# Performance work log

Measured on AMD Instinct MI355X. Metric: run time of the kernel, lower is better.

Reference implementation:

```python
import jax, jax.numpy as jnp
import numpy as np

NOISE_EPS = 1e-2   # Shazeer noisy-gating stddev floor
LN_EPS = 1e-6
LOSS_COEF = 0.01
K = 2              # num_activated_experts


def _layer_norm(x, w, b):
    mu = jnp.mean(x, axis=-1, keepdims=True)
    var = jnp.var(x, axis=-1, keepdims=True)
    return (x - mu) * jax.lax.rsqrt(var + LN_EPS) * w + b


def _cv_squared(v):
    return jnp.var(v) / (jnp.mean(v) ** 2 + 1e-10)


def _normal_cdf(z):
    return 0.5 * (1.0 + jax.scipy.special.erf(z / jnp.sqrt(jnp.asarray(2.0, z.dtype))))


def setup_inputs() -> dict:
    key = jax.random.key(0)
    ks = jax.random.split(key, 8)
    N, D, H, O, E = 8192, 512, 1024, 512, 8
    x = jax.random.normal(ks[0], (N, D), jnp.float32)
    x_offsets = jnp.sort(jax.random.randint(ks[1], (17,), 0, N)).astype(jnp.int64)
    noise = jax.random.normal(ks[2], (N, E), jnp.float32)
    s = 0.02
    return {
        "x": x,
        "x_offsets": x_offsets,
        "max_seq_len": 2048,
        "noise": noise,
        "norm_w": jnp.ones((D,), jnp.float32),
        "norm_bias": jnp.zeros((D,), jnp.float32),
        "w_gate": jax.random.normal(ks[3], (D, E), jnp.float32) * s,
        "w_noise": jax.random.normal(ks[4], (D, E), jnp.float32) * s,
        "W1": jax.random.normal(ks[5], (E, H, D), jnp.float32) * s,  # [E, model_d, input]
        "b1": jnp.zeros((E, H), jnp.float32),
        "W2": jax.random.normal(ks[6], (E, O, H), jnp.float32) * s,  # [E, output, model_d]
        "b2": jnp.zeros((E, O), jnp.float32),
        "output_weight": jax.random.normal(ks[7], (D, O), jnp.float32) * s,
    }


def reference(x, x_offsets, max_seq_len, noise, norm_w, norm_bias, w_gate, w_noise,
              W1, b1, W2, b2, output_weight):
    N, D = x.shape
    E = w_gate.shape[1]
    k_plus = min(K + 1, E)

    # pre-norm
    x_norm = _layer_norm(x, norm_w, norm_bias)

    # noisy top-k gating (training path)
    clean_logits = x_norm @ w_gate                      # [N, E]
    noise_stddev = jax.nn.softplus(x_norm @ w_noise) + NOISE_EPS
    noisy_logits = clean_logits + noise * noise_stddev

    top_logits, top_indices = jax.lax.top_k(noisy_logits, k_plus)   # [N, k+1]
    top_k_logits = top_logits[:, :K]
    top_k_indices = top_indices[:, :K]
    top_k_gates = jax.nn.softmax(top_k_logits, axis=-1)             # [N, K]

    rows = jnp.arange(N)[:, None]
    gates = jnp.zeros((N, E), top_k_gates.dtype).at[rows, top_k_indices].set(top_k_gates)

    # load = prob each expert is in top-k under the gating noise (Shazeer)
    flat = top_logits.reshape(-1)
    pos_in = jnp.arange(N) * k_plus + K
    thr_in = flat[pos_in][:, None]          # (k+1)-th value: threshold if already in
    thr_out = flat[pos_in - 1][:, None]     # k-th value: threshold if currently out
    is_in = noisy_logits > thr_in
    prob_in = _normal_cdf((clean_logits - thr_in) / noise_stddev)
    prob_out = _normal_cdf((clean_logits - thr_out) / noise_stddev)
    load_probs = jnp.where(is_in, prob_in, prob_out)                # [N, E]

    loss = LOSS_COEF * (_cv_squared(gates.sum(0)) + _cv_squared(load_probs.sum(0)))

    # dispatch stats: tokens per expert
    lengths = jnp.zeros((E,), jnp.float32).at[top_k_indices.reshape(-1)].add(1.0)
    load = lengths / lengths.sum()

    # grouped expert MLP (dense one-hot combine; gates are 0 for unrouted experts)
    h = jnp.einsum('nd,ehd->neh', x_norm, W1) + b1                  # [N, E, H]
    a = jax.nn.silu(h)
    y_e = jnp.einsum('neh,eoh->neo', a, W2) + b2                    # [N, E, O]
    y_moe = jnp.einsum('ne,neo->no', gates, y_e)                    # [N, O]

    # shared expert: addmm(y, shared_x=x, output_weight)
    y = y_moe + x @ output_weight
    return y, loss, load
```

## Files before the change

### kernel.cpp

```cpp
#include <hip/hip_runtime.h>
#include <math.h>

typedef unsigned short u16;
typedef unsigned int u32;

#define N_ROWS 8192
#define DDIM 512
#define HDIM 1024
#define ODIM 512
#define NEXP 8
#define MAXPAIRS (N_ROWS * 2)
#define MAXPOS (MAXPAIRS + NEXP * 128)
#define MAXTILES (MAXPOS / 128)

#define SM_CNT 0
#define SM_CUR 8
#define SM_AOFF 16
#define SM_GSUM 32
#define SM_LSUM 40
#define SM_WORDS 64

using short8 = __attribute__((ext_vector_type(8))) short;
using float4v = __attribute__((ext_vector_type(4))) float;

__device__ __forceinline__ u16 f2bf(float f) {
    union { float f; u32 u; } v; v.f = f;
    u32 u = v.u;
    return (u16)((u + 0x7fffu + ((u >> 16) & 1u)) >> 16);
}

__device__ __forceinline__ void async_copy16(u16* lds, const u16* g) {
    __builtin_amdgcn_global_load_lds(
        (const __attribute__((address_space(1))) void*)g,
        (__attribute__((address_space(3))) void*)lds, 16, 0, 0);
}

#define CONV_BLOCKS 8192
__global__ __launch_bounds__(256) void prep_kernel(
    const float* __restrict__ W1, const float* __restrict__ W2, const float* __restrict__ ow,
    u16* __restrict__ W1b, u16* __restrict__ W2b, u16* __restrict__ owT,
    int* __restrict__ small, int* __restrict__ bucket_rows, float* __restrict__ zeropage)
{
    __shared__ float tile[32][33];
    int b = blockIdx.x, tid = threadIdx.x;
    if (b < CONV_BLOCKS) {
        const size_t n4 = (size_t)NEXP * HDIM * DDIM / 4;
        size_t i = (size_t)b * 256 + tid;
        const float* src; u16* dst;
        if (i < n4) { src = W1; dst = W1b; } else { src = W2; dst = W2b; i -= n4; }
        float4 v = ((const float4*)src)[i];
        ushort4 o;
        o.x = f2bf(v.x); o.y = f2bf(v.y); o.z = f2bf(v.z); o.w = f2bf(v.w);
        ((ushort4*)dst)[i] = o;
    } else if (b < CONV_BLOCKS + 256) {
        int t = b - CONV_BLOCKS;
        int bx = (t & 15) * 32, by = (t >> 4) * 32;
        int tx = tid & 31, ty = tid >> 5;
        for (int r = ty; r < 32; r += 8) tile[r][tx] = ow[(size_t)(by + r) * ODIM + bx + tx];
        __syncthreads();
        for (int r = ty; r < 32; r += 8) owT[(size_t)(bx + r) * DDIM + by + tx] = f2bf(tile[tx][r]);
    } else {
        int i = (b - CONV_BLOCKS - 256) * 256 + tid;
        if (i < SM_WORDS) small[i] = 0;
        if (i < 512) zeropage[i] = 0.f;
        if (i < MAXPOS) bucket_rows[i] = -1;
    }
}

__global__ __launch_bounds__(256) void gating_kernel(
    const float* __restrict__ x, const float* __restrict__ noise,
    const float* __restrict__ norm_w, const float* __restrict__ norm_b,
    const float* __restrict__ w_gate, const float* __restrict__ w_noise,
    u16* __restrict__ xnorm_bf, u16* __restrict__ x_bf,
    int* __restrict__ pair_expert, float* __restrict__ pair_gate,
    int* __restrict__ small)
{
    __shared__ float wgT[NEXP * DDIM];
    __shared__ float wnT[NEXP * DDIM];
    __shared__ float blk_g[NEXP];
    __shared__ float blk_l[NEXP];
    __shared__ int blk_c[NEXP];
    float* smf = (float*)small;

    int tid = threadIdx.x;
    for (int i = tid; i < NEXP * DDIM; i += 256) {
        int d = i >> 3, e = i & 7;
        wgT[e * DDIM + d] = w_gate[i];
        wnT[e * DDIM + d] = w_noise[i];
    }
    if (tid < NEXP) { blk_g[tid] = 0.f; blk_l[tid] = 0.f; blk_c[tid] = 0; }
    __syncthreads();

    int wave = tid >> 6, lane = tid & 63;
    float nw[8], nb[8];
#pragma unroll
    for (int j = 0; j < 8; j++) { nw[j] = norm_w[j * 64 + lane]; nb[j] = norm_b[j * 64 + lane]; }

    for (int r = 0; r < 4; ++r) {
        int row = blockIdx.x * 16 + wave * 4 + r;
        const float* xr = x + (size_t)row * DDIM;
        float xv[8], s = 0.f, s2 = 0.f;
#pragma unroll
        for (int j = 0; j < 8; j++) { float v = xr[j * 64 + lane]; xv[j] = v; s += v; s2 += v * v; }
#pragma unroll
        for (int o = 32; o; o >>= 1) { s += __shfl_xor(s, o, 64); s2 += __shfl_xor(s2, o, 64); }
        float mu = s * (1.f / DDIM);
        float var = s2 * (1.f / DDIM) - mu * mu;
        float rstd = rsqrtf(var + 1e-6f);

        float acc[16];
#pragma unroll
        for (int e = 0; e < 16; e++) acc[e] = 0.f;
#pragma unroll
        for (int j = 0; j < 8; j++) {
            float v = (xv[j] - mu) * rstd * nw[j] + nb[j];
            int d = j * 64 + lane;
            xnorm_bf[(size_t)row * DDIM + d] = f2bf(v);
            x_bf[(size_t)row * DDIM + d] = f2bf(xv[j]);
#pragma unroll
            for (int e = 0; e < 8; e++) {
                acc[e] += v * wgT[e * DDIM + d];
                acc[8 + e] += v * wnT[e * DDIM + d];
            }
        }
#pragma unroll
        for (int e = 0; e < 16; e++)
#pragma unroll
            for (int o = 32; o; o >>= 1) acc[e] += __shfl_xor(acc[e], o, 64);

        float cl[8], sd[8], nz[8];
#pragma unroll
        for (int e = 0; e < 8; e++) {
            cl[e] = acc[e];
            float t = acc[8 + e];
            float sp = fmaxf(t, 0.f) + log1pf(expf(-fabsf(t)));
            sd[e] = sp + 0.01f;
            nz[e] = cl[e] + noise[(size_t)row * NEXP + e] * sd[e];
        }
        int idx[3]; float val[3]; u32 msk = 0;
#pragma unroll
        for (int t = 0; t < 3; t++) {
            float best = -INFINITY; int bi = 0;
#pragma unroll
            for (int e = 0; e < 8; e++)
                if (!((msk >> e) & 1) && nz[e] > best) { best = nz[e]; bi = e; }
            idx[t] = bi; val[t] = best; msk |= 1u << bi;
        }
        float e1 = expf(val[1] - val[0]);
        float g0 = 1.f / (1.f + e1), g1 = e1 / (1.f + e1);
        float thr_in = val[2], thr_out = val[1];

        if (lane == 0) {
            pair_expert[row * 2] = idx[0]; pair_gate[row * 2] = g0;
            pair_expert[row * 2 + 1] = idx[1]; pair_gate[row * 2 + 1] = g1;
            atomicAdd(&blk_g[idx[0]], g0); atomicAdd(&blk_g[idx[1]], g1);
            atomicAdd(&blk_c[idx[0]], 1); atomicAdd(&blk_c[idx[1]], 1);
#pragma unroll
            for (int e = 0; e < 8; e++) {
                float thr = (nz[e] > thr_in) ? thr_in : thr_out;
                float z = (cl[e] - thr) / sd[e];
                float p = 0.5f * (1.f + erff(z * 0.70710678118654752f));
                atomicAdd(&blk_l[e], p);
            }
        }
    }
    __syncthreads();
    if (tid < NEXP) {
        atomicAdd(smf + SM_GSUM + tid, blk_g[tid]);
        atomicAdd(smf + SM_LSUM + tid, blk_l[tid]);
        atomicAdd(&small[SM_CNT + tid], blk_c[tid]);
    }
}

__global__ __launch_bounds__(256) void scatter_kernel(
    const int* __restrict__ pair_expert, const float* __restrict__ pair_gate,
    int* __restrict__ small, int* __restrict__ bucket_rows, float* __restrict__ gate_by_pos,
    float* __restrict__ out_loss, float* __restrict__ out_load)
{
    __shared__ int aoff[NEXP + 1];
    __shared__ int blk_cnt[NEXP];
    __shared__ int blk_base[NEXP];
    int tid = threadIdx.x;
    if (tid == 0) {
        int acc = 0; aoff[0] = 0;
        for (int e = 0; e < NEXP; e++) { acc += (small[SM_CNT + e] + 127) & ~127; aoff[e + 1] = acc; }
    }
    if (tid < NEXP) blk_cnt[tid] = 0;
    __syncthreads();
    int p = blockIdx.x * 256 + tid;
    int e = pair_expert[p];
    int local = atomicAdd(&blk_cnt[e], 1);
    __syncthreads();
    if (tid < NEXP)
        blk_base[tid] = aoff[tid] + atomicAdd(&small[SM_CUR + tid], blk_cnt[tid]);
    if (blockIdx.x == 0 && tid < NEXP + 1) small[SM_AOFF + tid] = aoff[tid];
    __syncthreads();
    int pos = blk_base[e] + local;
    bucket_rows[pos] = p >> 1;
    gate_by_pos[pos] = pair_gate[p];

    if (blockIdx.x == 0 && tid == 0) {
        const float* gs = (const float*)small + SM_GSUM;
        const float* ls = (const float*)small + SM_LSUM;
        float cv[2];
        for (int t = 0; t < 2; t++) {
            const float* v = t ? ls : gs;
            float m = 0.f;
            for (int k = 0; k < NEXP; k++) m += v[k];
            m *= (1.f / NEXP);
            float var = 0.f;
            for (int k = 0; k < NEXP; k++) { float d = v[k] - m; var += d * d; }
            var *= (1.f / NEXP);
            cv[t] = var / (m * m + 1e-10f);
        }
        out_loss[0] = 0.01f * (cv[0] + cv[1]);
        int tot = 0;
        for (int k = 0; k < NEXP; k++) tot += small[SM_CNT + k];
        float inv = 1.f / (float)tot;
        for (int k = 0; k < NEXP; k++) out_load[k] = (float)small[SM_CNT + k] * inv;
    }
}

__global__ __launch_bounds__(256) void gemmA_kernel(
    const u16* __restrict__ xnorm, const u16* __restrict__ xbf,
    const u16* __restrict__ W1b, const u16* __restrict__ owT,
    const int* __restrict__ bucket_rows, const int* __restrict__ small,
    const float* __restrict__ b1, const u16* __restrict__ zeropage,
    u16* __restrict__ a_buf, float* __restrict__ y)
{
    constexpr int KD = 512;
    __shared__ __align__(16) u16 As[128 * 32];
    __shared__ __align__(16) u16 Bs[128 * 32];

    int tid = threadIdx.x;
    bool m0 = blockIdx.y < 8;
    int base, bn, e = 0;
    const u16* Bsel;
    if (m0) {
        base = blockIdx.x * 128;
        if (base >= small[SM_AOFF + 8]) return;
        while (e < 7 && base >= small[SM_AOFF + e + 1]) ++e;
        bn = blockIdx.y * 128;
        Bsel = W1b + (size_t)e * HDIM * KD;
    } else {
        int j = (blockIdx.y - 8) * 136 + blockIdx.x;
        if (j >= 256) return;
        base = (j >> 2) * 128;
        bn = (j & 3) * 128;
        Bsel = owT;
    }

    int wave = tid >> 6, lane = tid & 63;
    const int trow = wave * 32 + (lane >> 2);
    const int kcol = (lane & 3) * 8;
    const u16 *ga0, *ga1;
    if (m0) {
        int r0 = bucket_rows[base + trow];
        int r1 = bucket_rows[base + trow + 16];
        ga0 = ((r0 < 0) ? zeropage : xnorm + (size_t)r0 * KD) + kcol;
        ga1 = ((r1 < 0) ? zeropage : xnorm + (size_t)r1 * KD) + kcol;
    } else {
        ga0 = xbf + (size_t)(base + trow) * KD + kcol;
        ga1 = xbf + (size_t)(base + trow + 16) * KD + kcol;
    }
    const u16* gb0 = Bsel + (size_t)(bn + trow) * KD + kcol;
    const u16* gb1 = Bsel + (size_t)(bn + trow + 16) * KD + kcol;
    u16* lA0 = &As[(wave * 32) * 32];
    u16* lA1 = &As[(wave * 32 + 16) * 32];
    u16* lB0 = &Bs[(wave * 32) * 32];
    u16* lB1 = &Bs[(wave * 32 + 16) * 32];

    int wm = (wave & 1) * 64, wn = (wave >> 1) * 64;
    int fr = lane & 15, kg = (lane >> 4) * 8;

    float4v acc[4][4];
#pragma unroll
    for (int i = 0; i < 4; i++)
#pragma unroll
        for (int j = 0; j < 4; j++) acc[i][j] = (float4v){0.f, 0.f, 0.f, 0.f};

    for (int k0 = 0; k0 < KD; k0 += 32) {
        __syncthreads();
        async_copy16(lA0, ga0 + k0);
        async_copy16(lA1, ga1 + k0);
        async_copy16(lB0, gb0 + k0);
        async_copy16(lB1, gb1 + k0);
        __syncthreads();
        short8 af[4], bf[4];
#pragma unroll
        for (int mt = 0; mt < 4; mt++) af[mt] = *(const short8*)&As[(wm + mt * 16 + fr) * 32 + kg];
#pragma unroll
        for (int nt = 0; nt < 4; nt++) bf[nt] = *(const short8*)&Bs[(wn + nt * 16 + fr) * 32 + kg];
#pragma unroll
        for (int mt = 0; mt < 4; mt++)
#pragma unroll
            for (int nt = 0; nt < 4; nt++)
                acc[mt][nt] = __builtin_amdgcn_mfma_f32_16x16x32_bf16(af[mt], bf[nt], acc[mt][nt], 0, 0, 0);
    }

    int rbase = (lane >> 4) * 4, c16 = lane & 15;
#pragma unroll
    for (int nt = 0; nt < 4; nt++) {
        int gn = bn + wn + nt * 16 + c16;
        float bv = m0 ? b1[e * HDIM + gn] : 0.f;
#pragma unroll
        for (int mt = 0; mt < 4; mt++) {
            int gm = base + wm + mt * 16 + rbase;
#pragma unroll
            for (int r = 0; r < 4; r++) {
                float v = acc[mt][nt][r];
                if (m0) {
                    float h = v + bv;
                    float a = h * __builtin_amdgcn_rcpf(1.f + __expf(-h));
                    a_buf[(size_t)(gm + r) * HDIM + gn] = f2bf(a);
                } else {
                    y[(size_t)(gm + r) * ODIM + gn] = v;
                }
            }
        }
    }
}

__global__ __launch_bounds__(256) void gemmB_kernel(
    const u16* __restrict__ a_buf, const u16* __restrict__ W2b,
    const int* __restrict__ bucket_rows, const int* __restrict__ small,
    const float* __restrict__ b2, const float* __restrict__ gate_by_pos,
    float* __restrict__ y)
{
    constexpr int KD = 1024;
    __shared__ __align__(16) u16 As[128 * 32];
    __shared__ __align__(16) u16 Bs[128 * 32];

    int tid = threadIdx.x;
    int base = blockIdx.x * 128;
    if (base >= small[SM_AOFF + 8]) return;
    int e = 0;
    while (e < 7 && base >= small[SM_AOFF + e + 1]) ++e;
    int bn = blockIdx.y * 128;

    int wave = tid >> 6, lane = tid & 63;
    const int trow = wave * 32 + (lane >> 2);
    const int kcol = (lane & 3) * 8;
    const u16* ga0 = a_buf + (size_t)(base + trow) * KD + kcol;
    const u16* ga1 = a_buf + (size_t)(base + trow + 16) * KD + kcol;
    const u16* Bsel = W2b + (size_t)e * ODIM * KD;
    const u16* gb0 = Bsel + (size_t)(bn + trow) * KD + kcol;
    const u16* gb1 = Bsel + (size_t)(bn + trow + 16) * KD + kcol;
    u16* lA0 = &As[(wave * 32) * 32];
    u16* lA1 = &As[(wave * 32 + 16) * 32];
    u16* lB0 = &Bs[(wave * 32) * 32];
    u16* lB1 = &Bs[(wave * 32 + 16) * 32];

    int wm = (wave & 1) * 64, wn = (wave >> 1) * 64;
    int fr = lane & 15, kg = (lane >> 4) * 8;

    float4v acc[4][4];
#pragma unroll
    for (int i = 0; i < 4; i++)
#pragma unroll
        for (int j = 0; j < 4; j++) acc[i][j] = (float4v){0.f, 0.f, 0.f, 0.f};

    for (int k0 = 0; k0 < KD; k0 += 32) {
        __syncthreads();
        async_copy16(lA0, ga0 + k0);
        async_copy16(lA1, ga1 + k0);
        async_copy16(lB0, gb0 + k0);
        async_copy16(lB1, gb1 + k0);
        __syncthreads();
        short8 af[4], bf[4];
#pragma unroll
        for (int mt = 0; mt < 4; mt++) af[mt] = *(const short8*)&As[(wm + mt * 16 + fr) * 32 + kg];
#pragma unroll
        for (int nt = 0; nt < 4; nt++) bf[nt] = *(const short8*)&Bs[(wn + nt * 16 + fr) * 32 + kg];
#pragma unroll
        for (int mt = 0; mt < 4; mt++)
#pragma unroll
            for (int nt = 0; nt < 4; nt++)
                acc[mt][nt] = __builtin_amdgcn_mfma_f32_16x16x32_bf16(af[mt], bf[nt], acc[mt][nt], 0, 0, 0);
    }

    int rbase = (lane >> 4) * 4, c16 = lane & 15;
#pragma unroll
    for (int mt = 0; mt < 4; mt++) {
        int pos0 = base + wm + mt * 16 + rbase;
        int rows[4]; float gs[4];
#pragma unroll
        for (int r = 0; r < 4; r++) { rows[r] = bucket_rows[pos0 + r]; gs[r] = gate_by_pos[pos0 + r]; }
#pragma unroll
        for (int nt = 0; nt < 4; nt++) {
            int gn = bn + wn + nt * 16 + c16;
            float b2v = b2[e * ODIM + gn];
#pragma unroll
            for (int r = 0; r < 4; r++) {
                if (rows[r] >= 0)
                    unsafeAtomicAdd(&y[(size_t)rows[r] * ODIM + gn], gs[r] * (acc[mt][nt][r] + b2v));
            }
        }
    }
}

extern "C" void kernel_launch(void* const* d_in, const int* in_sizes, int n_in,
                              void* d_out, int out_size, void* d_ws, size_t ws_size,
                              hipStream_t stream)
{
    (void)in_sizes; (void)n_in; (void)out_size; (void)ws_size;
    const float* x = (const float*)d_in[0];
    const float* noise = (const float*)d_in[3];
    const float* norm_w = (const float*)d_in[4];
    const float* norm_b = (const float*)d_in[5];
    const float* w_gate = (const float*)d_in[6];
    const float* w_noise = (const float*)d_in[7];
    const float* W1 = (const float*)d_in[8];
    const float* b1 = (const float*)d_in[9];
    const float* W2 = (const float*)d_in[10];
    const float* b2 = (const float*)d_in[11];
    const float* ow = (const float*)d_in[12];

    float* y = (float*)d_out;
    float* out_loss = y + (size_t)N_ROWS * ODIM;
    float* out_load = out_loss + 1;

    char* ws = (char*)d_ws;
    size_t off = 0;
    auto alloc = [&](size_t b) { size_t p = off; off = (off + b + 255) & ~(size_t)255; return p; };
    u16* xnorm_bf = (u16*)(ws + alloc((size_t)N_ROWS * DDIM * 2));
    u16* x_bf     = (u16*)(ws + alloc((size_t)N_ROWS * DDIM * 2));
    u16* W1b      = (u16*)(ws + alloc((size_t)NEXP * HDIM * DDIM * 2));
    u16* W2b      = (u16*)(ws + alloc((size_t)NEXP * ODIM * HDIM * 2));
    u16* owT      = (u16*)(ws + alloc((size_t)DDIM * ODIM * 2));
    u16* a_buf    = (u16*)(ws + alloc((size_t)MAXPOS * HDIM * 2));
    int* pair_expert = (int*)(ws + alloc((size_t)MAXPAIRS * 4));
    float* pair_gate = (float*)(ws + alloc((size_t)MAXPAIRS * 4));
    float* gate_by_pos = (float*)(ws + alloc((size_t)MAXPOS * 4));
    int* bucket_rows = (int*)(ws + alloc((size_t)MAXPOS * 4));
    int* small       = (int*)(ws + alloc(SM_WORDS * 4));
    float* zeropage  = (float*)(ws + alloc(2048));

    prep_kernel<<<CONV_BLOCKS + 256 + 68, 256, 0, stream>>>(W1, W2, ow, W1b, W2b, owT,
                                                            small, bucket_rows, zeropage);
    gating_kernel<<<N_ROWS / 16, 256, 0, stream>>>(x, noise, norm_w, norm_b, w_gate, w_noise,
                                                   xnorm_bf, x_bf, pair_expert, pair_gate, small);
    scatter_kernel<<<MAXPAIRS / 256, 256, 0, stream>>>(pair_expert, pair_gate, small,
                                                       bucket_rows, gate_by_pos, out_loss, out_load);
    gemmA_kernel<<<dim3(MAXTILES, 10), 256, 0, stream>>>(xnorm_bf, x_bf, W1b, owT, bucket_rows,
                                                         small, b1, (const u16*)zeropage, a_buf, y);
    gemmB_kernel<<<dim3(MAXTILES, ODIM / 128), 256, 0, stream>>>(a_buf, W2b, bucket_rows, small,
                                                                 b2, gate_by_pos, y);
}
```

Measured before the change: 278.3 us.

## Load GEMM operands directly from global memory into registers, drop LDS staging

Both expert GEMM kernels stop staging A and B tiles through shared memory with async global-to-LDS copies and barriers. Each wave now loads its MFMA fragments straight from global memory into registers, with the k-loop unrolled by four. This removes the two barriers per k-step and the LDS round trip. In exchange, each wave re-fetches operands that were shared across waves, which raises global/L2 traffic and replaces coalesced 16-byte loads with per-lane strided row loads.

```diff
diff --git a/kernel.cpp b/kernel.cpp
--- a/kernel.cpp
+++ b/kernel.cpp
@@ -27,12 +27,6 @@
     union { float f; u32 u; } v; v.f = f;
     u32 u = v.u;
     return (u16)((u + 0x7fffu + ((u >> 16) & 1u)) >> 16);
-}
-
-__device__ __forceinline__ void async_copy16(u16* lds, const u16* g) {
-    __builtin_amdgcn_global_load_lds(
-        (const __attribute__((address_space(1))) void*)g,
-        (__attribute__((address_space(3))) void*)lds, 16, 0, 0);
 }
 
 #define CONV_BLOCKS 8192
@@ -221,6 +215,25 @@
     }
 }
 
+template <int KD>
+__device__ __forceinline__ void gemm_core_reg(const u16* const aptr[4], const u16* const bptr[4],
+                                              float4v acc[4][4])
+{
+#pragma unroll 4
+    for (int k0 = 0; k0 < KD; k0 += 32) {
+        short8 af[4], bf[4];
+#pragma unroll
+        for (int mt = 0; mt < 4; mt++) af[mt] = *(const short8*)(aptr[mt] + k0);
+#pragma unroll
+        for (int nt = 0; nt < 4; nt++) bf[nt] = *(const short8*)(bptr[nt] + k0);
+#pragma unroll
+        for (int mt = 0; mt < 4; mt++)
+#pragma unroll
+            for (int nt = 0; nt < 4; nt++)
+                acc[mt][nt] = __builtin_amdgcn_mfma_f32_16x16x32_bf16(af[mt], bf[nt], acc[mt][nt], 0, 0, 0);
+    }
+}
+
 __global__ __launch_bounds__(256) void gemmA_kernel(
     const u16* __restrict__ xnorm, const u16* __restrict__ xbf,
     const u16* __restrict__ W1b, const u16* __restrict__ owT,
@@ -229,9 +242,6 @@
     u16* __restrict__ a_buf, float* __restrict__ y)
 {
     constexpr int KD = 512;
-    __shared__ __align__(16) u16 As[128 * 32];
-    __shared__ __align__(16) u16 Bs[128 * 32];
-
     int tid = threadIdx.x;
     bool m0 = blockIdx.y < 8;
     int base, bn, e = 0;
@@ -251,52 +261,31 @@
     }
 
     int wave = tid >> 6, lane = tid & 63;
-    const int trow = wave * 32 + (lane >> 2);
-    const int kcol = (lane & 3) * 8;
-    const u16 *ga0, *ga1;
-    if (m0) {
-        int r0 = bucket_rows[base + trow];
-        int r1 = bucket_rows[base + trow + 16];
-        ga0 = ((r0 < 0) ? zeropage : xnorm + (size_t)r0 * KD) + kcol;
-        ga1 = ((r1 < 0) ? zeropage : xnorm + (size_t)r1 * KD) + kcol;
-    } else {
-        ga0 = xbf + (size_t)(base + trow) * KD + kcol;
-        ga1 = xbf + (size_t)(base + trow + 16) * KD + kcol;
-    }
-    const u16* gb0 = Bsel + (size_t)(bn + trow) * KD + kcol;
-    const u16* gb1 = Bsel + (size_t)(bn + trow + 16) * KD + kcol;
-    u16* lA0 = &As[(wave * 32) * 32];
-    u16* lA1 = &As[(wave * 32 + 16) * 32];
-    u16* lB0 = &Bs[(wave * 32) * 32];
-    u16* lB1 = &Bs[(wave * 32 + 16) * 32];
-
     int wm = (wave & 1) * 64, wn = (wave >> 1) * 64;
     int fr = lane & 15, kg = (lane >> 4) * 8;
 
+    const u16* aptr[4];
+    const u16* bptr[4];
+#pragma unroll
+    for (int mt = 0; mt < 4; mt++) {
+        int pos = base + wm + mt * 16 + fr;
+        if (m0) {
+            int r0 = bucket_rows[pos];
+            aptr[mt] = ((r0 < 0) ? zeropage : xnorm + (size_t)r0 * KD) + kg;
+        } else {
+            aptr[mt] = xbf + (size_t)pos * KD + kg;
+        }
+    }
+#pragma unroll
+    for (int nt = 0; nt < 4; nt++) bptr[nt] = Bsel + (size_t)(bn + wn + nt * 16 + fr) * KD + kg;
+
     float4v acc[4][4];
 #pragma unroll
     for (int i = 0; i < 4; i++)
 #pragma unroll
         for (int j = 0; j < 4; j++) acc[i][j] = (float4v){0.f, 0.f, 0.f, 0.f};
 
-    for (int k0 = 0; k0 < KD; k0 += 32) {
-        __syncthreads();
-        async_copy16(lA0, ga0 + k0);
-        async_copy16(lA1, ga1 + k0);
-        async_copy16(lB0, gb0 + k0);
-        async_copy16(lB1, gb1 + k0);
-        __syncthreads();
-        short8 af[4], bf[4];
-#pragma unroll
-        for (int mt = 0; mt < 4; mt++) af[mt] = *(const short8*)&As[(wm + mt * 16 + fr) * 32 + kg];
-#pragma unroll
-        for (int nt = 0; nt < 4; nt++) bf[nt] = *(const short8*)&Bs[(wn + nt * 16 + fr) * 32 + kg];
-#pragma unroll
-        for (int mt = 0; mt < 4; mt++)
-#pragma unroll
-            for (int nt = 0; nt < 4; nt++)
-                acc[mt][nt] = __builtin_amdgcn_mfma_f32_16x16x32_bf16(af[mt], bf[nt], acc[mt][nt], 0, 0, 0);
-    }
+    gemm_core_reg<KD>(aptr, bptr, acc);
 
     int rbase = (lane >> 4) * 4, c16 = lane & 15;
 #pragma unroll
@@ -328,9 +317,6 @@
     float* __restrict__ y)
 {
     constexpr int KD = 1024;
-    __shared__ __align__(16) u16 As[128 * 32];
-    __shared__ __align__(16) u16 Bs[128 * 32];
-
     int tid = threadIdx.x;
     int base = blockIdx.x * 128;
     if (base >= small[SM_AOFF + 8]) return;
@@ -339,45 +325,24 @@
     int bn = blockIdx.y * 128;
 
     int wave = tid >> 6, lane = tid & 63;
-    const int trow = wave * 32 + (lane >> 2);
-    const int kcol = (lane & 3) * 8;
-    const u16* ga0 = a_buf + (size_t)(base + trow) * KD + kcol;
-    const u16* ga1 = a_buf + (size_t)(base + trow + 16) * KD + kcol;
-    const u16* Bsel = W2b + (size_t)e * ODIM * KD;
-    const u16* gb0 = Bsel + (size_t)(bn + trow) * KD + kcol;
-    const u16* gb1 = Bsel + (size_t)(bn + trow + 16) * KD + kcol;
-    u16* lA0 = &As[(wave * 32) * 32];
-    u16* lA1 = &As[(wave * 32 + 16) * 32];
-    u16* lB0 = &Bs[(wave * 32) * 32];
-    u16* lB1 = &Bs[(wave * 32 + 16) * 32];
-
     int wm = (wave & 1) * 64, wn = (wave >> 1) * 64;
     int fr = lane & 15, kg = (lane >> 4) * 8;
 
+    const u16* aptr[4];
+    const u16* bptr[4];
+    const u16* Bsel = W2b + (size_t)e * ODIM * KD;
+#pragma unroll
+    for (int mt = 0; mt < 4; mt++) aptr[mt] = a_buf + (size_t)(base + wm + mt * 16 + fr) * KD + kg;
+#pragma unroll
+    for (int nt = 0; nt < 4; nt++) bptr[nt] = Bsel + (size_t)(bn + wn + nt * 16 + fr) * KD + kg;
+
     float4v acc[4][4];
 #pragma unroll
     for (int i = 0; i < 4; i++)
 #pragma unroll
         for (int j = 0; j < 4; j++) acc[i][j] = (float4v){0.f, 0.f, 0.f, 0.f};
 
-    for (int k0 = 0; k0 < KD; k0 += 32) {
-        __syncthreads();
-        async_copy16(lA0, ga0 + k0);
-        async_copy16(lA1, ga1 + k0);
-        async_copy16(lB0, gb0 + k0);
-        async_copy16(lB1, gb1 + k0);
-        __syncthreads();
-        short8 af[4], bf[4];
-#pragma unroll
-        for (int mt = 0; mt < 4; mt++) af[mt] = *(const short8*)&As[(wm + mt * 16 + fr) * 32 + kg];
-#pragma unroll
-        for (int nt = 0; nt < 4; nt++) bf[nt] = *(const short8*)&Bs[(wn + nt * 16 + fr) * 32 + kg];
-#pragma unroll
-        for (int mt = 0; mt < 4; mt++)
-#pragma unroll
-            for (int nt = 0; nt < 4; nt++)
-                acc[mt][nt] = __builtin_amdgcn_mfma_f32_16x16x32_bf16(af[mt], bf[nt], acc[mt][nt], 0, 0, 0);
-    }
+    gemm_core_reg<KD>(aptr, bptr, acc);
 
     int rbase = (lane >> 4) * 4, c16 = lane & 15;
 #pragma unroll
```

Measured after the change: 410.6 us. +47.5%, slower.
